# Kernel tuning notes

Measured on AMD Instinct MI355X. Metric: run time of the kernel, lower is better.

The kernel has to match this reference:

```python
import jax, jax.numpy as jnp
import numpy as np

N = 20000      # nodes
E = 500000     # edges (~25 neighbors/node)
G = 64         # graphs in batch
NF = 64        # num_features (node dim)
NG = 100       # num_gaussians (edge dim)
L = 6          # conv layers
FC = 128       # fc_feat_size
NFC = 3        # num_fc_layers - 1
EMB = 92       # KHOT embedding width
CUTOFF = 6.0
EPS = 1e-5


def setup_inputs() -> dict:
    key = jax.random.key(0)
    ks = jax.random.split(key, 16)
    s = 0.05
    inp = {}
    inp['atomic_numbers'] = jax.random.randint(ks[0], (N,), 0, 100, dtype=jnp.int32)
    inp['neighbors_index'] = jax.random.randint(ks[1], (2, E), 0, N, dtype=jnp.int32)
    inp['distances'] = jax.random.uniform(ks[2], (E,), dtype=jnp.float32) * CUTOFF
    inp['batch'] = jnp.sort(jax.random.randint(ks[3], (N,), 0, G, dtype=jnp.int32))
    # parameters
    inp['embedding'] = jax.random.normal(ks[4], (100, EMB), jnp.float32) * s
    inp['nuc_W'] = jax.random.normal(ks[5], (EMB, NF), jnp.float32) * s
    inp['nuc_b'] = jnp.zeros((NF,), jnp.float32)
    inp['conv_W'] = jax.random.normal(ks[6], (L, 2 * NF + NG, 2 * NF), jnp.float32) * s
    inp['conv_b'] = jnp.zeros((L, 2 * NF), jnp.float32)
    inp['bn_g'] = jnp.ones((L, 2 * NF), jnp.float32)
    inp['bn_b'] = jnp.zeros((L, 2 * NF), jnp.float32)
    inp['ln_g'] = jnp.ones((L, NF), jnp.float32)
    inp['ln_b'] = jnp.zeros((L, NF), jnp.float32)
    inp['fc1_W'] = jax.random.normal(ks[7], (NF, FC), jnp.float32) * s
    inp['fc1_b'] = jnp.zeros((FC,), jnp.float32)
    inp['fcs_W'] = jax.random.normal(ks[8], (NFC, FC, FC), jnp.float32) * s
    inp['fcs_b'] = jnp.zeros((NFC, FC), jnp.float32)
    inp['out_W'] = jax.random.normal(ks[9], (FC, 1), jnp.float32) * s
    inp['out_b'] = jnp.zeros((1,), jnp.float32)
    return inp


def reference(atomic_numbers, neighbors_index, distances, batch,
              embedding, nuc_W, nuc_b, conv_W, conv_b, bn_g, bn_b,
              ln_g, ln_b, fc1_W, fc1_b, fcs_W, fcs_b, out_W, out_b):
    # Gaussian smearing of edge distances -> [E, NG]
    offsets = jnp.linspace(0.0, CUTOFF, NG)
    coeff = -0.5 / (offsets[1] - offsets[0]) ** 2
    ef = jnp.exp(coeff * (distances[:, None] - offsets) ** 2)

    # atom k-hot embedding -> nuclear linear embedding: [N, NF]
    x = embedding[atomic_numbers] @ nuc_W + nuc_b

    src, dst = neighbors_index[0], neighbors_index[1]  # x_j = src, x_i = dst

    for l in range(L):
        # edge message: gather + concat + linear
        z = jnp.concatenate([x[dst], x[src], ef], axis=1) @ conv_W[l] + conv_b[l]
        # BatchNorm1d over edges (training-mode batch statistics, biased var)
        mu = z.mean(axis=0)
        var = jnp.mean((z - mu) ** 2, axis=0)
        z = (z - mu) / jnp.sqrt(var + EPS) * bn_g[l] + bn_b[l]
        z1, z2 = jnp.split(z, 2, axis=1)
        m = jax.nn.sigmoid(z1) * jax.nn.softplus(z2)  # [E, NF]
        # scatter-add aggregate to target nodes
        agg = jax.ops.segment_sum(m, dst, num_segments=N)
        # LayerNorm + residual + softplus
        mu2 = agg.mean(axis=-1, keepdims=True)
        var2 = jnp.mean((agg - mu2) ** 2, axis=-1, keepdims=True)
        h = (agg - mu2) / jnp.sqrt(var2 + EPS) * ln_g[l] + ln_b[l]
        x = jax.nn.softplus(h + x)

    # mean pool per graph
    counts = jnp.maximum(jax.ops.segment_sum(jnp.ones((N,), x.dtype), batch, num_segments=G), 1.0)
    mol = jax.ops.segment_sum(x, batch, num_segments=G) / counts[:, None]

    h = jax.nn.softplus(mol @ fc1_W + fc1_b)
    for i in range(NFC):
        h = jax.nn.softplus(h @ fcs_W[i] + fcs_b[i])
    y = h @ out_W + out_b  # [G, 1]
    return y
```

## Files before the change

kernel.cpp:

```cpp
#include <hip/hip_runtime.h>
#include <hip/hip_fp16.h>
#include <cmath>

#define NN 20000
#define EE 500000
#define GG 64
#define TS 8192
#define SW 4096
#define EPS 1e-5f

typedef unsigned long long u64a __attribute__((aligned(4)));

__device__ __forceinline__ float softplus_ref(float x) {
    return fmaxf(x, 0.f) + log1pf(__expf(-fabsf(x)));
}
__device__ __forceinline__ float softplus_fast(float x) {
    return fmaxf(x, 0.f) + __logf(1.0f + __expf(-fabsf(x)));
}
__device__ __forceinline__ float sigmoid_fast(float x) {
    return __builtin_amdgcn_rcpf(1.0f + __expf(-x));
}

__global__ void k_gtab(float* __restrict__ g) {
    int i = blockIdx.x * 256 + threadIdx.x;
    if (i >= TS * 100) return;
    int s = i / 100, k = i - 100 * s;
    float d = s * (6.0f / (TS - 1.0f));
    float o = k * (6.0f / 99.0f);
    float step = 6.0f / 99.0f;
    float coeff = -0.5f / (step * step);
    float df = d - o;
    g[i] = __expf(coeff * df * df);
}

__global__ void __launch_bounds__(256) k_build_T(
    const float* __restrict__ g, const float* __restrict__ convW,
    const float* __restrict__ convB, __half2* __restrict__ Tn) {
    int lane = threadIdx.x & 63;
    int wv = __builtin_amdgcn_readfirstlane(threadIdx.x >> 6);
    int l = blockIdx.y;
    int s0 = blockIdx.x * 16 + wv * 4;
    const float* w = convW + ((size_t)l * 228 + 128) * 128;
    const float* g0 = g + (size_t)s0 * 100;
    float b0 = convB[l * 128 + lane], b1 = convB[l * 128 + lane + 64];
    float2 a0 = {b0, b1}, a1 = {b0, b1}, a2 = {b0, b1}, a3 = {b0, b1};
#pragma unroll 4
    for (int k = 0; k < 100; k++) {
        float w0 = w[k * 128 + lane];
        float w1 = w[k * 128 + lane + 64];
        float ga = g0[k], gb = g0[100 + k], gc = g0[200 + k], gd = g0[300 + k];
        a0.x += ga * w0; a0.y += ga * w1;
        a1.x += gb * w0; a1.y += gb * w1;
        a2.x += gc * w0; a2.y += gc * w1;
        a3.x += gd * w0; a3.y += gd * w1;
    }
    Tn[((size_t)l * TS + s0 + 0) * 64 + lane] = __floats2half2_rn(a0.x, a0.y);
    Tn[((size_t)l * TS + s0 + 1) * 64 + lane] = __floats2half2_rn(a1.x, a1.y);
    Tn[((size_t)l * TS + s0 + 2) * 64 + lane] = __floats2half2_rn(a2.x, a2.y);
    Tn[((size_t)l * TS + s0 + 3) * 64 + lane] = __floats2half2_rn(a3.x, a3.y);
}

__global__ void k_prepW(const float* __restrict__ convW, float4* __restrict__ Wp) {
    int lane = threadIdx.x;
    int k = blockIdx.x;
    int l = blockIdx.y;
    const float* W1 = convW + ((size_t)l * 228 + k) * 128;
    const float* W2 = convW + ((size_t)l * 228 + 64 + k) * 128;
    Wp[((size_t)l * 64 + k) * 64 + lane] =
        make_float4(W1[lane], W1[lane + 64], W2[lane], W2[lane + 64]);
}

__global__ void k_embed(const int* __restrict__ an, const float* __restrict__ emb,
                        const float* __restrict__ W, const float* __restrict__ b,
                        float* __restrict__ x) {
    int c = threadIdx.x & 63, nl = threadIdx.x >> 6;
    int n = blockIdx.x * 4 + nl;
    if (n >= NN) return;
    const float* e = emb + (size_t)an[n] * 92;
    float acc = b[c];
#pragma unroll 4
    for (int k = 0; k < 92; k++) acc += e[k] * W[k * 64 + c];
    x[(size_t)n * 64 + c] = acc;
}

__global__ void k_hist(const int* __restrict__ dst, int* __restrict__ counts) {
    int e = blockIdx.x * 256 + threadIdx.x;
    if (e < EE) atomicAdd(&counts[dst[e]], 1);
}

__global__ void k_scan_local(const int* __restrict__ counts, int* __restrict__ rp,
                             int* __restrict__ bsum) {
    __shared__ int buf[1024];
    int b = blockIdx.x, tid = threadIdx.x;
    int i = b * 1024 + tid;
    int val = (i < NN) ? counts[i] : 0;
    buf[tid] = val;
    __syncthreads();
    for (int off = 1; off < 1024; off <<= 1) {
        int t = (tid >= off) ? buf[tid - off] : 0;
        __syncthreads();
        buf[tid] += t;
        __syncthreads();
    }
    if (i < NN) rp[i + 1] = buf[tid];
    if (tid == 1023) bsum[b] = buf[1023];
}

__global__ void k_scan_off(int* __restrict__ bsum, int nb) {
    if (threadIdx.x == 0) {
        int acc = 0;
        for (int b = 0; b < nb; b++) { int v = bsum[b]; bsum[b] = acc; acc += v; }
    }
}

__global__ void k_scan_add(int* __restrict__ rp, const int* __restrict__ bsum) {
    int b = blockIdx.x, tid = threadIdx.x;
    int i = b * 1024 + tid;
    if (i < NN) rp[i + 1] += bsum[b];
    if (b == 0 && tid == 0) rp[0] = 0;
}

__global__ void k_wsn(const int* __restrict__ rp, int* __restrict__ wsn) {
    int w = blockIdx.x * 256 + threadIdx.x;
    if (w >= SW) return;
    int e0 = (int)((long long)w * EE / SW);
    int lo = 0, hi = NN;
    while (lo + 1 < hi) {
        int mid = (lo + hi) >> 1;
        if (rp[mid] <= e0) lo = mid; else hi = mid;
    }
    wsn[w] = lo;
}

__global__ void k_scatter(const int* __restrict__ src, const int* __restrict__ dst,
                          const float* __restrict__ dist, const int* __restrict__ rp,
                          int* __restrict__ cursor, unsigned* __restrict__ ej) {
    int e = blockIdx.x * 256 + threadIdx.x;
    if (e < EE) {
        int d = dst[e];
        int p = atomicAdd(&cursor[d], 1);
        float t = dist[e] * ((TS - 1.0f) / 6.0f);
        int j = (int)(t + 0.5f);
        if (j > TS - 1) j = TS - 1;
        ej[rp[d] + p] = ((unsigned)src[e] << 13) | (unsigned)j;
    }
}

__global__ void __launch_bounds__(256) k_uv(const float* __restrict__ x,
                                            const float4* __restrict__ Wp,
                                            __half2* __restrict__ up, __half2* __restrict__ vp) {
    int lane = threadIdx.x & 63;
    int wv = __builtin_amdgcn_readfirstlane(threadIdx.x >> 6);
    int n0 = (blockIdx.x * 4 + wv) * 4;
    float xa = x[(size_t)(n0 + 0) * 64 + lane];
    float xb = x[(size_t)(n0 + 1) * 64 + lane];
    float xc = x[(size_t)(n0 + 2) * 64 + lane];
    float xd = x[(size_t)(n0 + 3) * 64 + lane];
    float2 ua = {0, 0}, ub = {0, 0}, uc = {0, 0}, ud = {0, 0};
    float2 va = {0, 0}, vb = {0, 0}, vc = {0, 0}, vd = {0, 0};
#pragma unroll 8
    for (int k = 0; k < 64; k++) {
        float4 w = Wp[k * 64 + lane];
        float ka = __uint_as_float(__builtin_amdgcn_readlane(__float_as_uint(xa), k));
        float kb = __uint_as_float(__builtin_amdgcn_readlane(__float_as_uint(xb), k));
        float kc = __uint_as_float(__builtin_amdgcn_readlane(__float_as_uint(xc), k));
        float kd = __uint_as_float(__builtin_amdgcn_readlane(__float_as_uint(xd), k));
        ua.x += ka * w.x; ua.y += ka * w.y; va.x += ka * w.z; va.y += ka * w.w;
        ub.x += kb * w.x; ub.y += kb * w.y; vb.x += kb * w.z; vb.y += kb * w.w;
        uc.x += kc * w.x; uc.y += kc * w.y; vc.x += kc * w.z; vc.y += kc * w.w;
        ud.x += kd * w.x; ud.y += kd * w.y; vd.x += kd * w.z; vd.y += kd * w.w;
    }
    up[(size_t)(n0 + 0) * 64 + lane] = __floats2half2_rn(ua.x, ua.y);
    up[(size_t)(n0 + 1) * 64 + lane] = __floats2half2_rn(ub.x, ub.y);
    up[(size_t)(n0 + 2) * 64 + lane] = __floats2half2_rn(uc.x, uc.y);
    up[(size_t)(n0 + 3) * 64 + lane] = __floats2half2_rn(ud.x, ud.y);
    vp[(size_t)(n0 + 0) * 64 + lane] = __floats2half2_rn(va.x, va.y);
    vp[(size_t)(n0 + 1) * 64 + lane] = __floats2half2_rn(vb.x, vb.y);
    vp[(size_t)(n0 + 2) * 64 + lane] = __floats2half2_rn(vc.x, vc.y);
    vp[(size_t)(n0 + 3) * 64 + lane] = __floats2half2_rn(vd.x, vd.y);
}

__global__ void __launch_bounds__(256) k_uvln(
    const float* __restrict__ accb,
    const float* __restrict__ lng, const float* __restrict__ lnb, int lp,
    const float* __restrict__ xin, float* __restrict__ xout,
    const float4* __restrict__ Wp,
    __half2* __restrict__ up, __half2* __restrict__ vp) {
    int lane = threadIdx.x & 63;
    int wv = __builtin_amdgcn_readfirstlane(threadIdx.x >> 6);
    int n0 = (blockIdx.x * 4 + wv) * 4;
    float lg = lng[lp * 64 + lane], lb = lnb[lp * 64 + lane];
    float xs[4];
#pragma unroll
    for (int j = 0; j < 4; j++) {
        int n = n0 + j;
        float a = accb[(size_t)n * 64 + lane];
        float xr = xin[(size_t)n * 64 + lane];
        float s = a;
#pragma unroll
        for (int off = 32; off; off >>= 1) s += __shfl_xor(s, off, 64);
        float mean = s * (1.0f / 64.0f);
        float e0v = a - mean;
        float vv2 = e0v * e0v;
#pragma unroll
        for (int off = 32; off; off >>= 1) vv2 += __shfl_xor(vv2, off, 64);
        float var = vv2 * (1.0f / 64.0f);
        float h = e0v * rsqrtf(var + EPS) * lg + lb;
        xs[j] = softplus_ref(h + xr);
        xout[(size_t)n * 64 + lane] = xs[j];
    }
    float xa = xs[0], xb = xs[1], xc = xs[2], xd = xs[3];
    float2 ua = {0, 0}, ub = {0, 0}, uc = {0, 0}, ud = {0, 0};
    float2 va = {0, 0}, vb = {0, 0}, vc = {0, 0}, vd = {0, 0};
#pragma unroll 8
    for (int k = 0; k < 64; k++) {
        float4 w = Wp[k * 64 + lane];
        float ka = __uint_as_float(__builtin_amdgcn_readlane(__float_as_uint(xa), k));
        float kb = __uint_as_float(__builtin_amdgcn_readlane(__float_as_uint(xb), k));
        float kc = __uint_as_float(__builtin_amdgcn_readlane(__float_as_uint(xc), k));
        float kd = __uint_as_float(__builtin_amdgcn_readlane(__float_as_uint(xd), k));
        ua.x += ka * w.x; ua.y += ka * w.y; va.x += ka * w.z; va.y += ka * w.w;
        ub.x += kb * w.x; ub.y += kb * w.y; vb.x += kb * w.z; vb.y += kb * w.w;
        uc.x += kc * w.x; uc.y += kc * w.y; vc.x += kc * w.z; vc.y += kc * w.w;
        ud.x += kd * w.x; ud.y += kd * w.y; vd.x += kd * w.z; vd.y += kd * w.w;
    }
    up[(size_t)(n0 + 0) * 64 + lane] = __floats2half2_rn(ua.x, ua.y);
    up[(size_t)(n0 + 1) * 64 + lane] = __floats2half2_rn(ub.x, ub.y);
    up[(size_t)(n0 + 2) * 64 + lane] = __floats2half2_rn(uc.x, uc.y);
    up[(size_t)(n0 + 3) * 64 + lane] = __floats2half2_rn(ud.x, ud.y);
    vp[(size_t)(n0 + 0) * 64 + lane] = __floats2half2_rn(va.x, va.y);
    vp[(size_t)(n0 + 1) * 64 + lane] = __floats2half2_rn(vb.x, vb.y);
    vp[(size_t)(n0 + 2) * 64 + lane] = __floats2half2_rn(vc.x, vc.y);
    vp[(size_t)(n0 + 3) * 64 + lane] = __floats2half2_rn(vd.x, vd.y);
}

#define GRP2(P, BODY)                                                        \
    {                                                                        \
        unsigned e[P];                                                       \
        _Pragma("unroll")                                                    \
        for (int t = 0; t < P; t++) {                                        \
            unsigned long long ep = *(const u64a*)&ej[idx + 2 * t];          \
            e[t] = slot ? (unsigned)(ep >> 32) : (unsigned)ep;               \
        }                                                                    \
        __half2 vh[P], th[P];                                                \
        _Pragma("unroll")                                                    \
        for (int t = 0; t < P; t++) {                                        \
            vh[t] = vp[(size_t)(e[t] >> 13) * 64 + hp];                      \
            th[t] = Tn[(size_t)(e[t] & 8191u) * 64 + hp];                    \
        }                                                                    \
        _Pragma("unroll")                                                    \
        for (int t = 0; t < P; t++) { BODY }                                 \
    }

#define STATS_BODY                                                           \
    float2 vv = __half22float2(vh[t]);                                       \
    float2 tt = __half22float2(th[t]);                                       \
    float z0 = uu.x + vv.x + tt.x;                                           \
    float z1 = uu.y + vv.y + tt.y;                                           \
    sx += z0; qx += z0 * z0; sy += z1; qy += z1 * z1;

#define AGG_BODY                                                             \
    __half2 vt = __hadd2(vh[t], th[t]);                                      \
    float2 f = __half22float2(vt);                                           \
    float z0 = fmaf(A1, f.x, C1);                                            \
    float z1 = fmaf(A2, f.y, C2);                                            \
    acc += sigmoid_fast(z0) * softplus_fast(z1);

__global__ void __launch_bounds__(256) k_stats_h(
    const __half2* __restrict__ up, const __half2* __restrict__ vp,
    const __half2* __restrict__ Tn, const unsigned* __restrict__ ej,
    const int* __restrict__ rp, const int* __restrict__ wsn,
    float* __restrict__ sums) {
    int lane = threadIdx.x & 63;
    int wv = __builtin_amdgcn_readfirstlane(threadIdx.x >> 6);
    int bid = blockIdx.x;
    int h = (bid >> 2) & 1;
    int r = ((bid >> 3) << 2) | (bid & 3);
    int slot = lane >> 5;
    int hp = h * 32 + (lane & 31);
    int w = r * 4 + wv;
    int e0 = (int)((long long)w * EE / SW);
    int e1 = (int)((long long)(w + 1) * EE / SW);
    int n = __builtin_amdgcn_readfirstlane(wsn[w]);
    int rend = __builtin_amdgcn_readfirstlane(rp[n + 1]);
    float sx = 0.f, sy = 0.f, qx = 0.f, qy = 0.f;
    int idx = e0;
    while (idx < e1) {
        while (idx >= rend) {
            ++n;
            rend = __builtin_amdgcn_readfirstlane(rp[n + 1]);
        }
        float2 uu = __half22float2(up[(size_t)n * 64 + hp]);
        int stop = (e1 < rend) ? e1 : rend;
        for (; idx + 16 <= stop; idx += 16) GRP2(8, STATS_BODY)
        if (idx + 8 <= stop) { GRP2(4, STATS_BODY) idx += 8; }
        if (idx + 4 <= stop) { GRP2(2, STATS_BODY) idx += 4; }
        if (idx + 2 <= stop) { GRP2(1, STATS_BODY) idx += 2; }
        if (idx < stop) {
            unsigned e = ej[idx];
            __half2 vh0 = vp[(size_t)(e >> 13) * 64 + hp];
            __half2 th0 = Tn[(size_t)(e & 8191u) * 64 + hp];
            float2 vv = __half22float2(vh0);
            float2 tt = __half22float2(th0);
            float z0 = uu.x + vv.x + tt.x;
            float z1 = uu.y + vv.y + tt.y;
            if (!slot) {
                sx += z0; qx += z0 * z0; sy += z1; qy += z1 * z1;
            }
            idx += 1;
        }
    }
    sx += __shfl_xor(sx, 32, 64); sy += __shfl_xor(sy, 32, 64);
    qx += __shfl_xor(qx, 32, 64); qy += __shfl_xor(qy, 32, 64);
    __shared__ float red[4][32][4];
    if (!slot) {
        float* rr = red[wv][lane & 31];
        rr[0] = sx; rr[1] = sy; rr[2] = qx; rr[3] = qy;
    }
    __syncthreads();
    if (wv == 0 && !slot) {
        for (int q = 1; q < 4; q++) {
            const float* rr = red[q][lane & 31];
            sx += rr[0]; sy += rr[1]; qx += rr[2]; qy += rr[3];
        }
        int c0 = hp;
        atomicAdd(&sums[c0], sx);
        atomicAdd(&sums[64 + c0], sy);
        atomicAdd(&sums[128 + c0], qx);
        atomicAdd(&sums[192 + c0], qy);
    }
}

__global__ void __launch_bounds__(256) k_aggh(
    const __half2* __restrict__ up, const __half2* __restrict__ vp,
    const __half2* __restrict__ Tn, const unsigned* __restrict__ ej,
    const int* __restrict__ rp, const float* __restrict__ sums,
    const float* __restrict__ bng, const float* __restrict__ bnb,
    int l, float* __restrict__ accbuf) {
    int lane = threadIdx.x & 63;
    int wv = __builtin_amdgcn_readfirstlane(threadIdx.x >> 6);
    int bid = blockIdx.x;
    int h = (bid >> 2) & 1;
    int r = ((bid >> 3) << 2) | (bid & 3);
    int slot = lane >> 5;
    int hp = h * 32 + (lane & 31);
    int i = r * 4 + wv;

    int c0 = hp;
    float mu1 = sums[c0] * (1.0f / EE);
    float var1 = sums[128 + c0] * (1.0f / EE) - mu1 * mu1;
    float A1 = rsqrtf(var1 + EPS) * bng[l * 128 + c0];
    float B1 = bnb[l * 128 + c0] - mu1 * A1;
    float mu2 = sums[64 + c0] * (1.0f / EE);
    float var2 = sums[192 + c0] * (1.0f / EE) - mu2 * mu2;
    float A2 = rsqrtf(var2 + EPS) * bng[l * 128 + 64 + c0];
    float B2 = bnb[l * 128 + 64 + c0] - mu2 * A2;

    float2 uu = __half22float2(up[(size_t)i * 64 + hp]);
    float C1 = fmaf(A1, uu.x, B1);
    float C2 = fmaf(A2, uu.y, B2);
    float acc = 0.f;
    int rs = __builtin_amdgcn_readfirstlane(rp[i]);
    int re = __builtin_amdgcn_readfirstlane(rp[i + 1]);
    int idx = rs;
    for (; idx + 16 <= re; idx += 16) GRP2(8, AGG_BODY)
    if (idx + 8 <= re) { GRP2(4, AGG_BODY) idx += 8; }
    if (idx + 4 <= re) { GRP2(2, AGG_BODY) idx += 4; }
    if (idx + 2 <= re) { GRP2(1, AGG_BODY) idx += 2; }
    if (idx < re) {
        unsigned e = ej[idx];
        __half2 vh0 = vp[(size_t)(e >> 13) * 64 + hp];
        __half2 th0 = Tn[(size_t)(e & 8191u) * 64 + hp];
        __half2 vt = __hadd2(vh0, th0);
        float2 f = __half22float2(vt);
        float z0 = fmaf(A1, f.x, C1);
        float z1 = fmaf(A2, f.y, C2);
        if (!slot) acc += sigmoid_fast(z0) * softplus_fast(z1);
    }
    acc += __shfl_xor(acc, 32, 64);
    if (!slot) accbuf[(size_t)i * 64 + hp] = acc;
}

__global__ void __launch_bounds__(256) k_lnfin(
    const float* __restrict__ accbuf,
    const float* __restrict__ lng, const float* __restrict__ lnb,
    int l, const float* __restrict__ xin, float* __restrict__ xout) {
    int lane = threadIdx.x & 63;
    int wv = __builtin_amdgcn_readfirstlane(threadIdx.x >> 6);
    int i = blockIdx.x * 4 + wv;
    float a = accbuf[(size_t)i * 64 + lane];
    float xr = xin[(size_t)i * 64 + lane];
    float s = a;
#pragma unroll
    for (int off = 32; off; off >>= 1) s += __shfl_xor(s, off, 64);
    float mean = s * (1.0f / 64.0f);
    float e0v = a - mean;
    float vv2 = e0v * e0v;
#pragma unroll
    for (int off = 32; off; off >>= 1) vv2 += __shfl_xor(vv2, off, 64);
    float var = vv2 * (1.0f / 64.0f);
    float h = e0v * rsqrtf(var + EPS) * lng[l * 64 + lane] + lnb[l * 64 + lane];
    xout[(size_t)i * 64 + lane] = softplus_ref(h + xr);
}

__global__ void k_gp(const int* __restrict__ batch, int* __restrict__ gp) {
    int g = threadIdx.x;
    if (g > GG) return;
    int lo = 0, hi = NN;
    while (lo < hi) {
        int mid = (lo + hi) >> 1;
        if (batch[mid] < g) lo = mid + 1; else hi = mid;
    }
    gp[g] = lo;
}

__global__ void k_pool2(const float* __restrict__ x, const int* __restrict__ gp,
                        float* __restrict__ mols) {
    int g = blockIdx.x;
    int lane = threadIdx.x & 63, slot = threadIdx.x >> 6;
    int s0 = gp[g], s1 = gp[g + 1];
    float acc = 0.f;
    for (int n = s0 + slot; n < s1; n += 4) acc += x[(size_t)n * 64 + lane];
    __shared__ float red[4][64];
    red[slot][lane] = acc;
    __syncthreads();
    if (slot == 0) {
        float a = red[0][lane] + red[1][lane] + red[2][lane] + red[3][lane];
        float cc = fmaxf((float)(s1 - s0), 1.0f);
        mols[g * 64 + lane] = a / cc;
    }
}

__global__ void k_mlp(const float* __restrict__ mols,
                      const float* __restrict__ fc1W, const float* __restrict__ fc1b,
                      const float* __restrict__ fcsW, const float* __restrict__ fcsb,
                      const float* __restrict__ outW, const float* __restrict__ outb,
                      float* __restrict__ y) {
    int g = blockIdx.x, t = threadIdx.x;
    __shared__ float m[64];
    __shared__ float h[128];
    __shared__ float rbuf[128];
    if (t < 64) m[t] = mols[g * 64 + t];
    __syncthreads();
    float a = fc1b[t];
#pragma unroll 16
    for (int k = 0; k < 64; k++) a += m[k] * fc1W[k * 128 + t];
    h[t] = softplus_ref(a);
    __syncthreads();
    for (int i = 0; i < 3; i++) {
        float b = fcsb[i * 128 + t];
#pragma unroll 16
        for (int k = 0; k < 128; k++) b += h[k] * fcsW[((size_t)i * 128 + k) * 128 + t];
        __syncthreads();
        h[t] = softplus_ref(b);
        __syncthreads();
    }
    rbuf[t] = h[t] * outW[t];
    __syncthreads();
    if (t < 64) {
        float s2 = rbuf[t] + rbuf[t + 64];
#pragma unroll
        for (int off = 32; off; off >>= 1) s2 += __shfl_xor(s2, off, 64);
        if (t == 0) y[g] = s2 + outb[0];
    }
}

extern "C" void kernel_launch(void* const* d_in, const int* in_sizes, int n_in,
                              void* d_out, int out_size, void* d_ws, size_t ws_size,
                              hipStream_t stream) {
    const int*   an    = (const int*)d_in[0];
    const int*   nbr   = (const int*)d_in[1];
    const float* dist  = (const float*)d_in[2];
    const int*   batch = (const int*)d_in[3];
    const float* emb   = (const float*)d_in[4];
    const float* nucW  = (const float*)d_in[5];
    const float* nucB  = (const float*)d_in[6];
    const float* convW = (const float*)d_in[7];
    const float* convB = (const float*)d_in[8];
    const float* bng   = (const float*)d_in[9];
    const float* bnb   = (const float*)d_in[10];
    const float* lng   = (const float*)d_in[11];
    const float* lnb   = (const float*)d_in[12];
    const float* fc1W  = (const float*)d_in[13];
    const float* fc1b  = (const float*)d_in[14];
    const float* fcsW  = (const float*)d_in[15];
    const float* fcsb  = (const float*)d_in[16];
    const float* outW  = (const float*)d_in[17];
    const float* outb  = (const float*)d_in[18];
    const int* srcI = nbr;
    const int* dstI = nbr + EE;

    char* base = (char*)d_ws;
    size_t off = 0;
    auto alloc = [&](size_t b) { size_t r = off; off += (b + 255) & ~(size_t)255; return r; };
    float*    gtab   = (float*)(base + alloc((size_t)TS * 100 * 4));
    __half2*  Tall   = (__half2*)(base + alloc((size_t)6 * TS * 64 * 4));
    float4*   Wp     = (float4*)(base + alloc((size_t)6 * 64 * 64 * 16));
    float*    x0     = (float*)(base + alloc((size_t)NN * 64 * 4));
    float*    x1     = (float*)(base + alloc((size_t)NN * 64 * 4));
    __half2*  up     = (__half2*)(base + alloc((size_t)NN * 64 * 4));
    __half2*  vp     = (__half2*)(base + alloc((size_t)NN * 64 * 4));
    float*    accb   = (float*)(base + alloc((size_t)NN * 64 * 4));
    float*    sums6  = (float*)(base + alloc((size_t)6 * 256 * 4));
    int*      counts = (int*)(base + alloc((size_t)NN * 4));
    int*      cursor = (int*)(base + alloc((size_t)NN * 4));
    int*      rp     = (int*)(base + alloc((size_t)(NN + 1) * 4));
    int*      bsum   = (int*)(base + alloc(64 * 4));
    unsigned* ej     = (unsigned*)(base + alloc((size_t)(EE + 64) * 4));
    int*      wsn    = (int*)(base + alloc((size_t)SW * 4));
    float*    mols   = (float*)(base + alloc((size_t)GG * 64 * 4));
    int*      gp     = (int*)(base + alloc((size_t)(GG + 1) * 4));

    hipMemsetAsync(counts, 0, (size_t)NN * 4, stream);
    hipMemsetAsync(cursor, 0, (size_t)NN * 4, stream);
    hipMemsetAsync(sums6, 0, (size_t)6 * 256 * 4, stream);

    k_gtab<<<(TS * 100 + 255) / 256, 256, 0, stream>>>(gtab);
    k_build_T<<<dim3(TS / 16, 6), 256, 0, stream>>>(gtab, convW, convB, Tall);
    k_prepW<<<dim3(64, 6), 64, 0, stream>>>(convW, Wp);
    k_embed<<<(NN + 3) / 4, 256, 0, stream>>>(an, emb, nucW, nucB, x0);
    k_hist<<<(EE + 255) / 256, 256, 0, stream>>>(dstI, counts);
    const int NB = (NN + 1023) / 1024;
    k_scan_local<<<NB, 1024, 0, stream>>>(counts, rp, bsum);
    k_scan_off<<<1, 64, 0, stream>>>(bsum, NB);
    k_scan_add<<<NB, 1024, 0, stream>>>(rp, bsum);
    k_wsn<<<SW / 256, 256, 0, stream>>>(rp, wsn);
    k_scatter<<<(EE + 255) / 256, 256, 0, stream>>>(srcI, dstI, dist, rp, cursor, ej);
    k_gp<<<1, 128, 0, stream>>>(batch, gp);

    float* xin = x0;
    float* xout = x1;
    for (int l = 0; l < 6; l++) {
        if (l == 0) {
            k_uv<<<NN / 16, 256, 0, stream>>>(xin, Wp, up, vp);
        } else {
            k_uvln<<<NN / 16, 256, 0, stream>>>(accb, lng, lnb, l - 1,
                                                xin, xout, Wp + (size_t)l * 64 * 64,
                                                up, vp);
            float* tmp = xin; xin = xout; xout = tmp;
        }
        const __half2* Tnl = Tall + (size_t)l * TS * 64;
        float* sums = sums6 + (size_t)l * 256;
        k_stats_h<<<2048, 256, 0, stream>>>(up, vp, Tnl, ej, rp, wsn, sums);
        k_aggh<<<10000, 256, 0, stream>>>(up, vp, Tnl, ej, rp, sums,
                                          bng, bnb, l, accb);
    }
    k_lnfin<<<NN / 4, 256, 0, stream>>>(accb, lng, lnb, 5, xin, xout);
    k_pool2<<<GG, 256, 0, stream>>>(xout, gp, mols);
    k_mlp<<<GG, 128, 0, stream>>>(mols, fc1W, fc1b, fcsW, fcsb, outW, outb, (float*)d_out);
}
```

Baseline: 832.2 us.

## Compute BatchNorm statistics from FP8-quantized v and T tables

Adds scaled FP8 (e4m3) copies of the per-node v projections and the per-distance edge table, written alongside the fp16 versions. The statistics pass now reads these 1-byte values, so each lane covers four channels and the old split into two channel halves disappears. It also doubles the number of edge-range work slices. This halves the gather bytes in the BN-stats pass, but adds extra stores and FP8 decode work, and BatchNorm mean and variance lose precision.

```diff
diff --git a/kernel.cpp b/kernel.cpp
--- a/kernel.cpp
+++ b/kernel.cpp
@@ -1,12 +1,13 @@
 #include <hip/hip_runtime.h>
 #include <hip/hip_fp16.h>
+#include <hip/hip_fp8.h>
 #include <cmath>
 
 #define NN 20000
 #define EE 500000
 #define GG 64
 #define TS 8192
-#define SW 4096
+#define SW 8192
 #define EPS 1e-5f
 
 typedef unsigned long long u64a __attribute__((aligned(4)));
@@ -19,6 +20,15 @@
 }
 __device__ __forceinline__ float sigmoid_fast(float x) {
     return __builtin_amdgcn_rcpf(1.0f + __expf(-x));
+}
+__device__ __forceinline__ unsigned char f8e(float x) {
+    __hip_fp8_e4m3 t(16.0f * x);
+    return (unsigned char)t.__x;
+}
+__device__ __forceinline__ float f8d(unsigned b) {
+    __hip_fp8_e4m3 v;
+    v.__x = (__hip_fp8_storage_t)b;
+    return (float)v;
 }
 
 __global__ void k_gtab(float* __restrict__ g) {
@@ -35,7 +45,8 @@
 
 __global__ void __launch_bounds__(256) k_build_T(
     const float* __restrict__ g, const float* __restrict__ convW,
-    const float* __restrict__ convB, __half2* __restrict__ Tn) {
+    const float* __restrict__ convB, __half2* __restrict__ Tn,
+    uchar2* __restrict__ Tn8) {
     int lane = threadIdx.x & 63;
     int wv = __builtin_amdgcn_readfirstlane(threadIdx.x >> 6);
     int l = blockIdx.y;
@@ -58,6 +69,10 @@
     Tn[((size_t)l * TS + s0 + 1) * 64 + lane] = __floats2half2_rn(a1.x, a1.y);
     Tn[((size_t)l * TS + s0 + 2) * 64 + lane] = __floats2half2_rn(a2.x, a2.y);
     Tn[((size_t)l * TS + s0 + 3) * 64 + lane] = __floats2half2_rn(a3.x, a3.y);
+    Tn8[((size_t)l * TS + s0 + 0) * 64 + lane] = make_uchar2(f8e(a0.x), f8e(a0.y));
+    Tn8[((size_t)l * TS + s0 + 1) * 64 + lane] = make_uchar2(f8e(a1.x), f8e(a1.y));
+    Tn8[((size_t)l * TS + s0 + 2) * 64 + lane] = make_uchar2(f8e(a2.x), f8e(a2.y));
+    Tn8[((size_t)l * TS + s0 + 3) * 64 + lane] = make_uchar2(f8e(a3.x), f8e(a3.y));
 }
 
 __global__ void k_prepW(const float* __restrict__ convW, float4* __restrict__ Wp) {
@@ -148,7 +163,8 @@
 
 __global__ void __launch_bounds__(256) k_uv(const float* __restrict__ x,
                                             const float4* __restrict__ Wp,
-                                            __half2* __restrict__ up, __half2* __restrict__ vp) {
+                                            __half2* __restrict__ up, __half2* __restrict__ vp,
+                                            uchar2* __restrict__ vp8) {
     int lane = threadIdx.x & 63;
     int wv = __builtin_amdgcn_readfirstlane(threadIdx.x >> 6);
     int n0 = (blockIdx.x * 4 + wv) * 4;
@@ -178,6 +194,10 @@
     vp[(size_t)(n0 + 1) * 64 + lane] = __floats2half2_rn(vb.x, vb.y);
     vp[(size_t)(n0 + 2) * 64 + lane] = __floats2half2_rn(vc.x, vc.y);
     vp[(size_t)(n0 + 3) * 64 + lane] = __floats2half2_rn(vd.x, vd.y);
+    vp8[(size_t)(n0 + 0) * 64 + lane] = make_uchar2(f8e(va.x), f8e(va.y));
+    vp8[(size_t)(n0 + 1) * 64 + lane] = make_uchar2(f8e(vb.x), f8e(vb.y));
+    vp8[(size_t)(n0 + 2) * 64 + lane] = make_uchar2(f8e(vc.x), f8e(vc.y));
+    vp8[(size_t)(n0 + 3) * 64 + lane] = make_uchar2(f8e(vd.x), f8e(vd.y));
 }
 
 __global__ void __launch_bounds__(256) k_uvln(
@@ -185,7 +205,8 @@
     const float* __restrict__ lng, const float* __restrict__ lnb, int lp,
     const float* __restrict__ xin, float* __restrict__ xout,
     const float4* __restrict__ Wp,
-    __half2* __restrict__ up, __half2* __restrict__ vp) {
+    __half2* __restrict__ up, __half2* __restrict__ vp,
+    uchar2* __restrict__ vp8) {
     int lane = threadIdx.x & 63;
     int wv = __builtin_amdgcn_readfirstlane(threadIdx.x >> 6);
     int n0 = (blockIdx.x * 4 + wv) * 4;
@@ -232,6 +253,110 @@
     vp[(size_t)(n0 + 1) * 64 + lane] = __floats2half2_rn(vb.x, vb.y);
     vp[(size_t)(n0 + 2) * 64 + lane] = __floats2half2_rn(vc.x, vc.y);
     vp[(size_t)(n0 + 3) * 64 + lane] = __floats2half2_rn(vd.x, vd.y);
+    vp8[(size_t)(n0 + 0) * 64 + lane] = make_uchar2(f8e(va.x), f8e(va.y));
+    vp8[(size_t)(n0 + 1) * 64 + lane] = make_uchar2(f8e(vb.x), f8e(vb.y));
+    vp8[(size_t)(n0 + 2) * 64 + lane] = make_uchar2(f8e(vc.x), f8e(vc.y));
+    vp8[(size_t)(n0 + 3) * 64 + lane] = make_uchar2(f8e(vd.x), f8e(vd.y));
+}
+
+#define SGRP8(P)                                                             \
+    {                                                                        \
+        unsigned e[P];                                                       \
+        _Pragma("unroll")                                                    \
+        for (int t = 0; t < P; t++) {                                        \
+            unsigned long long ep = *(const u64a*)&ej[idx + 2 * t];          \
+            e[t] = slot ? (unsigned)(ep >> 32) : (unsigned)ep;               \
+        }                                                                    \
+        unsigned vr[P], tr[P];                                               \
+        _Pragma("unroll")                                                    \
+        for (int t = 0; t < P; t++) {                                        \
+            vr[t] = vq8[(size_t)(e[t] >> 13) * 32 + q];                      \
+            tr[t] = tq8[(size_t)(e[t] & 8191u) * 32 + q];                    \
+        }                                                                    \
+        _Pragma("unroll")                                                    \
+        for (int t = 0; t < P; t++) {                                        \
+            float z00 = u0 + f8d(vr[t] & 255u) + f8d(tr[t] & 255u);          \
+            float z10 = u1 + f8d((vr[t] >> 8) & 255u) + f8d((tr[t] >> 8) & 255u); \
+            float z01 = u2 + f8d((vr[t] >> 16) & 255u) + f8d((tr[t] >> 16) & 255u); \
+            float z11 = u3 + f8d(vr[t] >> 24) + f8d(tr[t] >> 24);            \
+            sza += z00; qza += z00 * z00; sya += z10; qya += z10 * z10;      \
+            szb += z01; qzb += z01 * z01; syb += z11; qyb += z11 * z11;      \
+        }                                                                    \
+    }
+
+__global__ void __launch_bounds__(256) k_stats8(
+    const __half2* __restrict__ up, const unsigned* __restrict__ vq8,
+    const unsigned* __restrict__ tq8, const unsigned* __restrict__ ej,
+    const int* __restrict__ rp, const int* __restrict__ wsn,
+    float* __restrict__ sums) {
+    int lane = threadIdx.x & 63;
+    int wv = __builtin_amdgcn_readfirstlane(threadIdx.x >> 6);
+    int slot = lane >> 5, q = lane & 31;
+    int w = blockIdx.x * 4 + wv;
+    int e0 = (int)((long long)w * EE / SW);
+    int e1 = (int)((long long)(w + 1) * EE / SW);
+    int n = __builtin_amdgcn_readfirstlane(wsn[w]);
+    int rend = __builtin_amdgcn_readfirstlane(rp[n + 1]);
+    float sza = 0, szb = 0, sya = 0, syb = 0;
+    float qza = 0, qzb = 0, qya = 0, qyb = 0;
+    float u0 = 0, u1 = 0, u2 = 0, u3 = 0;
+    int idx = e0;
+    while (idx < e1) {
+        while (idx >= rend) {
+            ++n;
+            rend = __builtin_amdgcn_readfirstlane(rp[n + 1]);
+        }
+        {
+            uint2 uw = *(const uint2*)&up[(size_t)n * 64 + 2 * q];
+            float2 fa = __half22float2(*(const __half2*)&uw.x);
+            float2 fb = __half22float2(*(const __half2*)&uw.y);
+            u0 = 16.0f * fa.x; u1 = 16.0f * fa.y;
+            u2 = 16.0f * fb.x; u3 = 16.0f * fb.y;
+        }
+        int stop = (e1 < rend) ? e1 : rend;
+        for (; idx + 16 <= stop; idx += 16) SGRP8(8)
+        if (idx + 8 <= stop) { SGRP8(4) idx += 8; }
+        if (idx + 4 <= stop) { SGRP8(2) idx += 4; }
+        if (idx + 2 <= stop) { SGRP8(1) idx += 2; }
+        if (idx < stop) {
+            unsigned e = ej[idx];
+            unsigned vr = vq8[(size_t)(e >> 13) * 32 + q];
+            unsigned tr = tq8[(size_t)(e & 8191u) * 32 + q];
+            float z00 = u0 + f8d(vr & 255u) + f8d(tr & 255u);
+            float z10 = u1 + f8d((vr >> 8) & 255u) + f8d((tr >> 8) & 255u);
+            float z01 = u2 + f8d((vr >> 16) & 255u) + f8d((tr >> 16) & 255u);
+            float z11 = u3 + f8d(vr >> 24) + f8d(tr >> 24);
+            if (!slot) {
+                sza += z00; qza += z00 * z00; sya += z10; qya += z10 * z10;
+                szb += z01; qzb += z01 * z01; syb += z11; qyb += z11 * z11;
+            }
+            idx += 1;
+        }
+    }
+    sza += __shfl_xor(sza, 32, 64); szb += __shfl_xor(szb, 32, 64);
+    sya += __shfl_xor(sya, 32, 64); syb += __shfl_xor(syb, 32, 64);
+    qza += __shfl_xor(qza, 32, 64); qzb += __shfl_xor(qzb, 32, 64);
+    qya += __shfl_xor(qya, 32, 64); qyb += __shfl_xor(qyb, 32, 64);
+    __shared__ float red[4][32][8];
+    if (!slot) {
+        float* rr = red[wv][q];
+        rr[0] = sza; rr[1] = szb; rr[2] = sya; rr[3] = syb;
+        rr[4] = qza; rr[5] = qzb; rr[6] = qya; rr[7] = qyb;
+    }
+    __syncthreads();
+    if (wv == 0 && !slot) {
+        for (int r = 1; r < 4; r++) {
+            const float* rr = red[r][q];
+            sza += rr[0]; szb += rr[1]; sya += rr[2]; syb += rr[3];
+            qza += rr[4]; qzb += rr[5]; qya += rr[6]; qyb += rr[7];
+        }
+        int cA = 2 * q, cB = 2 * q + 1;
+        const float s1 = 1.0f / 16.0f, s2 = 1.0f / 256.0f;
+        atomicAdd(&sums[cA], sza * s1);        atomicAdd(&sums[cB], szb * s1);
+        atomicAdd(&sums[64 + cA], sya * s1);   atomicAdd(&sums[64 + cB], syb * s1);
+        atomicAdd(&sums[128 + cA], qza * s2);  atomicAdd(&sums[128 + cB], qzb * s2);
+        atomicAdd(&sums[192 + cA], qya * s2);  atomicAdd(&sums[192 + cB], qyb * s2);
+    }
 }
 
 #define GRP2(P, BODY)                                                        \
@@ -252,84 +377,12 @@
         for (int t = 0; t < P; t++) { BODY }                                 \
     }
 
-#define STATS_BODY                                                           \
-    float2 vv = __half22float2(vh[t]);                                       \
-    float2 tt = __half22float2(th[t]);                                       \
-    float z0 = uu.x + vv.x + tt.x;                                           \
-    float z1 = uu.y + vv.y + tt.y;                                           \
-    sx += z0; qx += z0 * z0; sy += z1; qy += z1 * z1;
-
 #define AGG_BODY                                                             \
     __half2 vt = __hadd2(vh[t], th[t]);                                      \
     float2 f = __half22float2(vt);                                           \
     float z0 = fmaf(A1, f.x, C1);                                            \
     float z1 = fmaf(A2, f.y, C2);                                            \
     acc += sigmoid_fast(z0) * softplus_fast(z1);
-
-__global__ void __launch_bounds__(256) k_stats_h(
-    const __half2* __restrict__ up, const __half2* __restrict__ vp,
-    const __half2* __restrict__ Tn, const unsigned* __restrict__ ej,
-    const int* __restrict__ rp, const int* __restrict__ wsn,
-    float* __restrict__ sums) {
-    int lane = threadIdx.x & 63;
-    int wv = __builtin_amdgcn_readfirstlane(threadIdx.x >> 6);
-    int bid = blockIdx.x;
-    int h = (bid >> 2) & 1;
-    int r = ((bid >> 3) << 2) | (bid & 3);
-    int slot = lane >> 5;
-    int hp = h * 32 + (lane & 31);
-    int w = r * 4 + wv;
-    int e0 = (int)((long long)w * EE / SW);
-    int e1 = (int)((long long)(w + 1) * EE / SW);
-    int n = __builtin_amdgcn_readfirstlane(wsn[w]);
-    int rend = __builtin_amdgcn_readfirstlane(rp[n + 1]);
-    float sx = 0.f, sy = 0.f, qx = 0.f, qy = 0.f;
-    int idx = e0;
-    while (idx < e1) {
-        while (idx >= rend) {
-            ++n;
-            rend = __builtin_amdgcn_readfirstlane(rp[n + 1]);
-        }
-        float2 uu = __half22float2(up[(size_t)n * 64 + hp]);
-        int stop = (e1 < rend) ? e1 : rend;
-        for (; idx + 16 <= stop; idx += 16) GRP2(8, STATS_BODY)
-        if (idx + 8 <= stop) { GRP2(4, STATS_BODY) idx += 8; }
-        if (idx + 4 <= stop) { GRP2(2, STATS_BODY) idx += 4; }
-        if (idx + 2 <= stop) { GRP2(1, STATS_BODY) idx += 2; }
-        if (idx < stop) {
-            unsigned e = ej[idx];
-            __half2 vh0 = vp[(size_t)(e >> 13) * 64 + hp];
-            __half2 th0 = Tn[(size_t)(e & 8191u) * 64 + hp];
-            float2 vv = __half22float2(vh0);
-            float2 tt = __half22float2(th0);
-            float z0 = uu.x + vv.x + tt.x;
-            float z1 = uu.y + vv.y + tt.y;
-            if (!slot) {
-                sx += z0; qx += z0 * z0; sy += z1; qy += z1 * z1;
-            }
-            idx += 1;
-        }
-    }
-    sx += __shfl_xor(sx, 32, 64); sy += __shfl_xor(sy, 32, 64);
-    qx += __shfl_xor(qx, 32, 64); qy += __shfl_xor(qy, 32, 64);
-    __shared__ float red[4][32][4];
-    if (!slot) {
-        float* rr = red[wv][lane & 31];
-        rr[0] = sx; rr[1] = sy; rr[2] = qx; rr[3] = qy;
-    }
-    __syncthreads();
-    if (wv == 0 && !slot) {
-        for (int q = 1; q < 4; q++) {
-            const float* rr = red[q][lane & 31];
-            sx += rr[0]; sy += rr[1]; qx += rr[2]; qy += rr[3];
-        }
-        int c0 = hp;
-        atomicAdd(&sums[c0], sx);
-        atomicAdd(&sums[64 + c0], sy);
-        atomicAdd(&sums[128 + c0], qx);
-        atomicAdd(&sums[192 + c0], qy);
-    }
-}
 
 __global__ void __launch_bounds__(256) k_aggh(
     const __half2* __restrict__ up, const __half2* __restrict__ vp,
@@ -495,11 +548,13 @@
     auto alloc = [&](size_t b) { size_t r = off; off += (b + 255) & ~(size_t)255; return r; };
     float*    gtab   = (float*)(base + alloc((size_t)TS * 100 * 4));
     __half2*  Tall   = (__half2*)(base + alloc((size_t)6 * TS * 64 * 4));
+    uchar2*   Tall8  = (uchar2*)(base + alloc((size_t)6 * TS * 64 * 2));
     float4*   Wp     = (float4*)(base + alloc((size_t)6 * 64 * 64 * 16));
     float*    x0     = (float*)(base + alloc((size_t)NN * 64 * 4));
     float*    x1     = (float*)(base + alloc((size_t)NN * 64 * 4));
     __half2*  up     = (__half2*)(base + alloc((size_t)NN * 64 * 4));
     __half2*  vp     = (__half2*)(base + alloc((size_t)NN * 64 * 4));
+    uchar2*   vp8    = (uchar2*)(base + alloc((size_t)NN * 64 * 2));
     float*    accb   = (float*)(base + alloc((size_t)NN * 64 * 4));
     float*    sums6  = (float*)(base + alloc((size_t)6 * 256 * 4));
     int*      counts = (int*)(base + alloc((size_t)NN * 4));
@@ -516,7 +571,7 @@
     hipMemsetAsync(sums6, 0, (size_t)6 * 256 * 4, stream);
 
     k_gtab<<<(TS * 100 + 255) / 256, 256, 0, stream>>>(gtab);
-    k_build_T<<<dim3(TS / 16, 6), 256, 0, stream>>>(gtab, convW, convB, Tall);
+    k_build_T<<<dim3(TS / 16, 6), 256, 0, stream>>>(gtab, convW, convB, Tall, Tall8);
     k_prepW<<<dim3(64, 6), 64, 0, stream>>>(convW, Wp);
     k_embed<<<(NN + 3) / 4, 256, 0, stream>>>(an, emb, nucW, nucB, x0);
     k_hist<<<(EE + 255) / 256, 256, 0, stream>>>(dstI, counts);
@@ -532,16 +587,18 @@
     float* xout = x1;
     for (int l = 0; l < 6; l++) {
         if (l == 0) {
-            k_uv<<<NN / 16, 256, 0, stream>>>(xin, Wp, up, vp);
+            k_uv<<<NN / 16, 256, 0, stream>>>(xin, Wp, up, vp, vp8);
         } else {
             k_uvln<<<NN / 16, 256, 0, stream>>>(accb, lng, lnb, l - 1,
                                                 xin, xout, Wp + (size_t)l * 64 * 64,
-                                                up, vp);
+                                                up, vp, vp8);
             float* tmp = xin; xin = xout; xout = tmp;
         }
         const __half2* Tnl = Tall + (size_t)l * TS * 64;
+        const unsigned* Tnl8 = (const unsigned*)(Tall8 + (size_t)l * TS * 64);
         float* sums = sums6 + (size_t)l * 256;
-        k_stats_h<<<2048, 256, 0, stream>>>(up, vp, Tnl, ej, rp, wsn, sums);
+        k_stats8<<<2048, 256, 0, stream>>>(up, (const unsigned*)vp8, Tnl8,
+                                           ej, rp, wsn, sums);
         k_aggh<<<10000, 256, 0, stream>>>(up, vp, Tnl, ej, rp, sums,
                                           bng, bnb, l, accb);
     }
```

Result: slower. 1.248 ms (+49.9%).
